# Performance work log

Hardware: AMD Instinct MI355X
Metric: run time of the kernel (lower is better)

The kernel has to match this reference:

```python
import jax, jax.numpy as jnp
import numpy as np

B, P, K = 8, 2048, 20          # graphs, points per graph, fps samples per graph
N, M = B * P, B * K            # total points, total fps points
C_IN, C_OUT = 64, 128
EPS = 1e-5                     # BatchNorm eps (torch default)


def _linear(x, W, b):
    return x @ W.T + b


def _bn(x, g, b):
    # training-mode BatchNorm1d: batch stats over rows (biased variance)
    m = jnp.mean(x, axis=0)
    v = jnp.var(x, axis=0)
    return g * (x - m) * jax.lax.rsqrt(v + EPS) + b


def _mlp(x, W1, b1, g1, be1, W2, b2, g2, be2):
    h = jax.nn.relu(_bn(_linear(x, W1, b1), g1, be1))
    return jax.nn.relu(_bn(_linear(h, W2, b2), g2, be2))


def setup_inputs() -> dict:
    key = jax.random.key(0)
    ks = jax.random.split(key, 16)
    rng = np.random.default_rng(0)
    # sorted FPS indices: 20 distinct points per graph (matches indices.sort())
    fps = np.sort(rng.choice(P, size=(B, K), replace=False), axis=1)
    fps = fps + np.arange(B)[:, None] * P

    s = 0.05
    inp = {
        "x": jax.random.normal(ks[0], (N, C_IN), jnp.float32),
        "pos": jax.random.normal(ks[1], (N, 3), jnp.float32),
        # q/k/v projections
        "Wq": jax.random.normal(ks[2], (C_OUT, C_IN)) * s, "bq": jnp.zeros((C_OUT,)),
        "Wk": jax.random.normal(ks[3], (C_OUT, C_IN)) * s, "bk": jnp.zeros((C_OUT,)),
        "Wv": jax.random.normal(ks[4], (C_OUT, C_IN)) * s, "bv": jnp.zeros((C_OUT,)),
        # pos MLP: Linear(3,C) BN ReLU Linear(C,C) BN ReLU
        "pW1": jax.random.normal(ks[5], (C_OUT, 3)) * s, "pb1": jnp.zeros((C_OUT,)),
        "pg1": jnp.ones((C_OUT,)), "pbe1": jnp.zeros((C_OUT,)),
        "pW2": jax.random.normal(ks[6], (C_OUT, C_OUT)) * s, "pb2": jnp.zeros((C_OUT,)),
        "pg2": jnp.ones((C_OUT,)), "pbe2": jnp.zeros((C_OUT,)),
        # attn MLP: Linear(C,C) BN ReLU Linear(C,C) BN ReLU
        "aW1": jax.random.normal(ks[7], (C_OUT, C_OUT)) * s, "ab1": jnp.zeros((C_OUT,)),
        "ag1": jnp.ones((C_OUT,)), "abe1": jnp.zeros((C_OUT,)),
        "aW2": jax.random.normal(ks[8], (C_OUT, C_OUT)) * s, "ab2": jnp.zeros((C_OUT,)),
        "ag2": jnp.ones((C_OUT,)), "abe2": jnp.zeros((C_OUT,)),
        "fps_idx": jnp.asarray(fps.reshape(-1), jnp.int32),
        "batch": jnp.repeat(jnp.arange(B, dtype=jnp.int32), P),
    }
    return inp


def reference(x, pos, Wq, bq, Wk, bk, Wv, bv,
              pW1, pb1, pg1, pbe1, pW2, pb2, pg2, pbe2,
              aW1, ab1, ag1, abe1, aW2, ab2, ag2, abe2,
              fps_idx, batch):
    # --- FPS gather + knn(k=1, batched) ---
    fps_pos = pos[fps_idx]                          # [M,3]
    pos_b = pos.reshape(B, P, 3)
    fpos_b = fps_pos.reshape(B, K, 3)
    d2 = jnp.sum((pos_b[:, :, None, :] - fpos_b[:, None, :, :]) ** 2, -1)  # [B,P,K]
    nn_local = jnp.argmin(d2, axis=-1)              # [B,P] nearest fps per point
    e1 = (nn_local + jnp.arange(B)[:, None] * K).reshape(-1)  # [N] global fps idx
    ek1 = 1.0 / (1.0 + 5.0 * jnp.min(d2, axis=-1).reshape(-1))  # [N]

    # --- scatter-mean of kernel-weighted x/pos onto fps nodes ---
    seg = jax.ops.segment_sum
    cnt = jnp.maximum(seg(jnp.ones((N,), x.dtype), e1, num_segments=M), 1.0)[:, None]
    fps_x = seg(ek1[:, None] * x, e1, num_segments=M) / cnt       # [M,C_IN]
    fps_pos = seg(ek1[:, None] * pos, e1, num_segments=M) / cnt   # [M,3]

    # --- q/k/v projections ---
    x_q = _linear(x, Wq, bq)        # [N,C]
    x_k = _linear(fps_x, Wk, bk)    # [M,C]
    x_v = _linear(fps_x, Wv, bv)    # [M,C]

    # --- all-pairs (local point, global fps-in-same-graph) edges: E = N*K ---
    rel = (pos_b[:, :, None, :] - fps_pos.reshape(B, K, 3)[:, None, :, :])
    rel = rel.reshape(N * K, 3)                                   # [E,3]
    delta = _mlp(rel, pW1, pb1, pg1, pbe1, pW2, pb2, pg2, pbe2)   # [E,C]

    qmk = (x_q.reshape(B, P, 1, C_OUT) - x_k.reshape(B, 1, K, C_OUT))
    qmk = qmk.reshape(N * K, C_OUT)                               # [E,C]
    alpha = _mlp(qmk + delta, aW1, ab1, ag1, abe1, aW2, ab2, ag2, abe2)
    # segment softmax over each local point's K edges, per channel
    alpha = jax.nn.softmax(alpha.reshape(B, P, K, C_OUT), axis=2)

    vpd = x_v.reshape(B, 1, K, C_OUT) + delta.reshape(B, P, K, C_OUT)
    out = jnp.sum(vpd * alpha, axis=2).reshape(N, C_OUT)          # scatter-add
    return out
```

## Files before the change

kernel.cpp:

```cpp
#include <hip/hip_runtime.h>
#include <hip/hip_bf16.h>
#include <stdint.h>

#define B_ 8
#define P_ 2048
#define K_ 20
#define N_ (B_*P_)
#define M_ (B_*K_)
#define C 128
#define E_ (N_*K_)
#define EPS_ 1e-5f

typedef unsigned short u16;
typedef unsigned int u32;
typedef __attribute__((ext_vector_type(8))) short short8;
typedef __attribute__((ext_vector_type(4))) float floatx4;

__device__ __forceinline__ float bf2f(u16 u){
    union { u32 i; float f; } v; v.i = ((u32)u) << 16; return v.f;
}
__device__ __forceinline__ u16 f2bf(float f){
    union { float f; u32 i; } v; v.f = f;
    u32 r = ((v.i >> 16) & 1u) + 0x7fffu;
    return (u16)((v.i + r) >> 16);
}
__device__ __forceinline__ u32 pkbf(float a, float b){
    union { __hip_bfloat162 h; u32 u; } cv;
    cv.h = __float22bfloat162_rn(make_float2(a, b));
    return cv.u;
}

__global__ __launch_bounds__(256)
void prep_weights(const float* __restrict__ Wq, const float* __restrict__ bq,
                  const float* __restrict__ Wk, const float* __restrict__ bk,
                  const float* __restrict__ aW1, const float* __restrict__ ab1,
                  const float* __restrict__ pW2, const float* __restrict__ aW2,
                  const float* __restrict__ Wv,
                  float* __restrict__ CqT, float* __restrict__ CkT,
                  float* __restrict__ dq, float* __restrict__ dk,
                  float* __restrict__ WvT,
                  u16* __restrict__ Wb0, u16* __restrict__ Wb1, u16* __restrict__ Wb2)
{
    int tid = threadIdx.x, blk = blockIdx.x;
    if (blk < 32) {
        int idx = blk*256 + tid; int o = idx >> 6, i = idx & 63;
        float s = 0.f;
        for (int cc = 0; cc < 128; ++cc) s = fmaf(aW1[o*128+cc], Wq[cc*64+i], s);
        CqT[i*128 + o] = s;
    } else if (blk < 64) {
        int idx = (blk-32)*256 + tid; int o = idx >> 6, i = idx & 63;
        float s = 0.f;
        for (int cc = 0; cc < 128; ++cc) s = fmaf(aW1[o*128+cc], Wk[cc*64+i], s);
        CkT[i*128 + o] = s;
    } else if (blk == 64) {
        if (tid < 128) {
            float s = ab1[tid];
            for (int cc = 0; cc < 128; ++cc) s = fmaf(aW1[tid*128+cc], bq[cc], s);
            dq[tid] = s;
        } else {
            int o = tid - 128;
            float s = 0.f;
            for (int cc = 0; cc < 128; ++cc) s = fmaf(aW1[o*128+cc], bk[cc], s);
            dk[o] = s;
        }
    } else if (blk == 68) {
        for (int idx = tid; idx < 8192; idx += 256) {
            int o = idx >> 6, i = idx & 63;
            WvT[i*128 + o] = Wv[idx];
        }
    } else {
        const float* src = (blk == 65) ? pW2 : (blk == 66) ? aW1 : aW2;
        u16* dst = (blk == 65) ? Wb0 : (blk == 66) ? Wb1 : Wb2;
        for (int s = tid; s < 2048; s += 256) {
            int ln = s & 63, ks = (s >> 6) & 3, ct = s >> 8;
            int Ls = ln & 15, qs = ln >> 4;
            const float* sp = src + (ct*16+Ls)*C + ks*32 + qs*8;
            #pragma unroll
            for (int j = 0; j < 8; ++j) dst[s*8+j] = f2bf(sp[j]);
        }
    }
}

__global__ __launch_bounds__(256)
void knn_scatter(const float* __restrict__ pos, const float* __restrict__ x,
                 const int* __restrict__ fps_idx, float* __restrict__ gacc,
                 float* __restrict__ posmom)
{
    __shared__ float fpos[K_][3];
    __shared__ float accL[K_*68];
    __shared__ int   skb[64];
    __shared__ float sek[64];
    int tid = threadIdx.x;
    int b = blockIdx.x >> 5;
    if (tid < K_*3) {
        int k = tid / 3, d = tid - k*3;
        fpos[k][d] = pos[fps_idx[b*K_+k]*3 + d];
    }
    for (int i = tid; i < K_*68; i += 256) accL[i] = 0.f;
    __syncthreads();

    int wbase = blockIdx.x*64;
    if (tid < 64) {
        int p = wbase + tid;
        float px = pos[p*3], py = pos[p*3+1], pz = pos[p*3+2];
        float best = 1e30f; int kb = 0;
        #pragma unroll
        for (int k = 0; k < K_; ++k) {
            float dx = px - fpos[k][0], dy = py - fpos[k][1], dz = pz - fpos[k][2];
            float d2 = dx*dx + dy*dy + dz*dz;
            if (d2 < best) { best = d2; kb = k; }
        }
        float ek = 1.0f / (1.0f + 5.0f*best);
        skb[tid] = kb; sek[tid] = ek;
        atomicAdd(&accL[kb*68 + 0], 1.0f);
        atomicAdd(&accL[kb*68 + 1], ek*px);
        atomicAdd(&accL[kb*68 + 2], ek*py);
        atomicAdd(&accL[kb*68 + 3], ek*pz);

        float mom[9] = {px,py,pz, px*px,px*py,px*pz, py*py,py*pz, pz*pz};
        #pragma unroll
        for (int i = 0; i < 9; ++i) {
            float v = mom[i];
            v += __shfl_xor(v,32); v += __shfl_xor(v,16); v += __shfl_xor(v,8);
            v += __shfl_xor(v,4);  v += __shfl_xor(v,2);  v += __shfl_xor(v,1);
            mom[i] = v;
        }
        if (tid == 0) {
            #pragma unroll
            for (int i = 0; i < 9; ++i) atomicAdd(&posmom[b*9+i], mom[i]);
        }
    }
    __syncthreads();

    int w = tid >> 6, lane = tid & 63;
    #pragma unroll
    for (int jj = 0; jj < 16; ++jj) {
        int j = w*16 + jj;
        int   kbj = skb[j];
        float ekj = sek[j];
        float xvv = x[(size_t)(wbase+j)*64 + lane];
        atomicAdd(&accL[kbj*68 + 4 + lane], ekj*xvv);
    }
    __syncthreads();
    for (int i = tid; i < K_*68; i += 256)
        atomicAdd(&gacc[b*K_*68 + i], accL[i]);
}

__global__ __launch_bounds__(128)
void proj_m(float* __restrict__ gacc, const float* __restrict__ CkT,
            const float* __restrict__ dk, const float* __restrict__ WvT,
            const float* __restrict__ bv, float* __restrict__ Ak2,
            float* __restrict__ xv)
{
    __shared__ float sfx[68];
    int m = blockIdx.x, o = threadIdx.x;
    if (o < 68) {
        float c = gacc[m*68];
        float inv = 1.0f / (c > 1.f ? c : 1.f);
        float vdiv = (o >= 1) ? gacc[m*68+o]*inv : c;
        sfx[o] = vdiv;
        if (o >= 1) gacc[m*68+o] = vdiv;
    }
    __syncthreads();
    float a = dk[o], v = bv[o];
    for (int i = 0; i < 64; ++i) {
        float xi = sfx[4+i];
        a = fmaf(CkT[i*128+o], xi, a);
        v = fmaf(WvT[i*128+o], xi, v);
    }
    Ak2[m*C+o] = a; xv[m*C+o] = v;
}

__global__ __launch_bounds__(256)
void bn1_prep(const float* __restrict__ gacc, const float* __restrict__ posmom,
              const float* __restrict__ pW1, const float* __restrict__ pb1,
              const float* __restrict__ pg1, const float* __restrict__ pbe1,
              float* __restrict__ w3)
{
    __shared__ float sF[8][3], sG[8][6];
    __shared__ float S1[3], S2[6];
    int t = threadIdx.x;
    if (t < 8) {
        float F0=0,F1=0,F2=0,G0=0,G1=0,G2=0,G3=0,G4=0,G5=0;
        for (int k = 0; k < K_; ++k) {
            const float* f = gacc + (t*K_+k)*68 + 1;
            float x=f[0], y=f[1], z=f[2];
            F0+=x; F1+=y; F2+=z;
            G0+=x*x; G1+=x*y; G2+=x*z; G3+=y*y; G4+=y*z; G5+=z*z;
        }
        sF[t][0]=F0; sF[t][1]=F1; sF[t][2]=F2;
        sG[t][0]=G0; sG[t][1]=G1; sG[t][2]=G2; sG[t][3]=G3; sG[t][4]=G4; sG[t][5]=G5;
    }
    __syncthreads();
    if (t == 0) {
        float s1[3]={0,0,0}, s2[6]={0,0,0,0,0,0};
        for (int b = 0; b < 8; ++b) {
            const float* pm = posmom + b*9;
            float Ax=pm[0],Ay=pm[1],Az=pm[2];
            float Fx=sF[b][0],Fy=sF[b][1],Fz=sF[b][2];
            s1[0] += (float)K_*Ax - (float)P_*Fx;
            s1[1] += (float)K_*Ay - (float)P_*Fy;
            s1[2] += (float)K_*Az - (float)P_*Fz;
            s2[0] += (float)K_*pm[3] - 2.f*Ax*Fx + (float)P_*sG[b][0];
            s2[1] += (float)K_*pm[4] - Ax*Fy - Ay*Fx + (float)P_*sG[b][1];
            s2[2] += (float)K_*pm[5] - Ax*Fz - Az*Fx + (float)P_*sG[b][2];
            s2[3] += (float)K_*pm[6] - 2.f*Ay*Fy + (float)P_*sG[b][3];
            s2[4] += (float)K_*pm[7] - Ay*Fz - Az*Fy + (float)P_*sG[b][4];
            s2[5] += (float)K_*pm[8] - 2.f*Az*Fz + (float)P_*sG[b][5];
        }
        for (int i = 0; i < 3; ++i) S1[i] = s1[i];
        for (int i = 0; i < 6; ++i) S2[i] = s2[i];
    }
    __syncthreads();
    if (t < 128) {
        float w0=pW1[t*3], w1=pW1[t*3+1], w2=pW1[t*3+2], bb=pb1[t];
        float wS1 = w0*S1[0] + w1*S1[1] + w2*S1[2];
        float wS2w = w0*w0*S2[0] + w1*w1*S2[3] + w2*w2*S2[5]
                   + 2.f*(w0*w1*S2[1] + w0*w2*S2[2] + w1*w2*S2[4]);
        const float invE = 1.0f/(float)E_;
        float m1  = wS1*invE + bb;
        float Ez2 = (wS2w + 2.f*bb*wS1)*invE + bb*bb;
        float var = Ez2 - m1*m1;
        float sc = pg1[t] * rsqrtf(var + EPS_);
        float sh = pbe1[t] - m1*sc;
        w3[0*128+t] = w0*sc; w3[1*128+t] = w1*sc;
        w3[2*128+t] = w2*sc; w3[3*128+t] = bb*sc + sh;
    }
}

__global__ __launch_bounds__(256)
void proj_q(const float* __restrict__ x, const float* __restrict__ CqT,
            const float* __restrict__ dq, float* __restrict__ Aq2)
{
    __shared__ float xs[512];
    int tid = threadIdx.x;
    int p0 = blockIdx.x*8;
    const float* xp = x + (size_t)p0*64;
    for (int i = tid; i < 512; i += 256) xs[i] = xp[i];
    __syncthreads();
    int g = tid >> 7, o = tid & 127;
    const float* xb = xs + g*256;
    float d = dq[o];
    float a0=d, a1=d, a2=d, a3=d;
    #pragma unroll 4
    for (int i = 0; i < 64; ++i) {
        float w = CqT[i*128 + o];
        a0 = fmaf(w, xb[i],       a0);
        a1 = fmaf(w, xb[64+i],    a1);
        a2 = fmaf(w, xb[128+i],   a2);
        a3 = fmaf(w, xb[192+i],   a3);
    }
    int pb = p0 + g*4;
    Aq2[(size_t)(pb+0)*C + o] = a0;
    Aq2[(size_t)(pb+1)*C + o] = a1;
    Aq2[(size_t)(pb+2)*C + o] = a2;
    Aq2[(size_t)(pb+3)*C + o] = a3;
}

template<int MODE>
__global__ __launch_bounds__(256)
void gemm_fused(const u16* __restrict__ zin, u16* __restrict__ zout,
                const u16* __restrict__ Wbf,
                const float* __restrict__ statsin, const float* __restrict__ g,
                const float* __restrict__ be,
                const float* __restrict__ w3, const float* __restrict__ bias,
                const float* __restrict__ rowq, const float* __restrict__ rowk,
                const float* __restrict__ pos, const float* __restrict__ gacc,
                float* __restrict__ stats32)
{
    __shared__ float s_stat[2][C];
    __shared__ float saff[5*C];

    int tid = threadIdx.x;
    const int wave = tid >> 6, lane = tid & 63;
    const int L = lane & 15, q = lane >> 4;

    ((float*)s_stat)[tid] = 0.f;
    if constexpr (MODE == 0) {
        for (int i = tid; i < 512; i += 256) saff[i] = w3[i];
        if (tid < C) saff[512+tid] = bias[tid];
    } else {
        if (tid < C) {
            float s = 0.f, sq = 0.f;
            for (int r = 0; r < 32; ++r) {
                s  += statsin[r*256 + tid];
                sq += statsin[r*256 + 128 + tid];
            }
            float mean = s*(1.0f/E_), var = sq*(1.0f/E_) - mean*mean;
            float sc = g[tid] * rsqrtf(var + EPS_);
            saff[tid] = sc; saff[C+tid] = be[tid] - mean*sc;
        }
        if constexpr (MODE == 2) {
            if (tid >= 128) saff[2*C + tid - 128] = bias[tid - 128];
        }
    }
    __syncthreads();

    int tbs[2];
    tbs[0] = (blockIdx.x*8 + wave)*16;
    tbs[1] = (blockIdx.x*8 + wave + 4)*16;

    short8 An[2][4];
    float rr0[2], rr1[2], rr2[2];
    #pragma unroll
    for (int tt = 0; tt < 2; ++tt) {
        if constexpr (MODE != 0) {
            const u16* ap = zin + (size_t)(tbs[tt] + L)*C + q*8;
            An[tt][0] = *(const short8*)ap;
            An[tt][1] = *(const short8*)(ap + 32);
            An[tt][2] = *(const short8*)(ap + 64);
            An[tt][3] = *(const short8*)(ap + 96);
        } else {
            unsigned e = (unsigned)(tbs[tt] + L);
            unsigned p = e / 20u; int k = (int)(e - p*20u);
            int m = (int)(p >> 11)*20 + k;
            const float* fp = gacc + m*68 + 1;
            rr0[tt] = pos[p*3]   - fp[0];
            rr1[tt] = pos[p*3+1] - fp[1];
            rr2[tt] = pos[p*3+2] - fp[2];
        }
    }

    floatx4 acc[2][8];
    #pragma unroll
    for (int tt = 0; tt < 2; ++tt)
        #pragma unroll
        for (int ct = 0; ct < 8; ++ct) acc[tt][ct] = (floatx4){0.f,0.f,0.f,0.f};

    #pragma unroll
    for (int ks = 0; ks < 4; ++ks) {
        int ch0 = ks*32 + q*8;
        short8 bfr[8];
        #pragma unroll
        for (int ct = 0; ct < 8; ++ct)
            bfr[ct] = *(const short8*)(Wbf + ((ct*4+ks)*64 + lane)*8);
        #pragma unroll
        for (int tt = 0; tt < 2; ++tt) {
            union { short8 s8; u32 u[4]; } af;
            if constexpr (MODE == 0) {
                #pragma unroll
                for (int jj = 0; jj < 4; ++jj) {
                    int c0 = ch0 + jj*2, c1 = ch0 + jj*2 + 1;
                    float f0 = fmaf(saff[c0], rr0[tt], fmaf(saff[C+c0], rr1[tt],
                               fmaf(saff[2*C+c0], rr2[tt], saff[3*C+c0])));
                    float f1 = fmaf(saff[c1], rr0[tt], fmaf(saff[C+c1], rr1[tt],
                               fmaf(saff[2*C+c1], rr2[tt], saff[3*C+c1])));
                    f0 = f0 > 0.f ? f0 : 0.f;
                    f1 = f1 > 0.f ? f1 : 0.f;
                    af.u[jj] = pkbf(f0, f1);
                }
            } else {
                short8 ar = An[tt][ks];
                #pragma unroll
                for (int jj = 0; jj < 4; ++jj) {
                    int c0 = ch0 + jj*2, c1 = ch0 + jj*2 + 1;
                    float f0 = fmaf(bf2f((u16)ar[jj*2]),   saff[c0], saff[C+c0]);
                    float f1 = fmaf(bf2f((u16)ar[jj*2+1]), saff[c1], saff[C+c1]);
                    f0 = f0 > 0.f ? f0 : 0.f;
                    f1 = f1 > 0.f ? f1 : 0.f;
                    af.u[jj] = pkbf(f0, f1);
                }
            }
            #pragma unroll
            for (int ct = 0; ct < 8; ++ct)
                acc[tt][ct] = __builtin_amdgcn_mfma_f32_16x16x32_bf16(af.s8, bfr[ct], acc[tt][ct], 0, 0, 0);
        }
    }

    float ssum[8], ssq[8];
    #pragma unroll
    for (int i = 0; i < 8; ++i) { ssum[i] = 0.f; ssq[i] = 0.f; }

    #pragma unroll
    for (int tt = 0; tt < 2; ++tt) {
        const int tilebase = tbs[tt];
        int pp[4], mm[4];
        if constexpr (MODE == 1) {
            #pragma unroll
            for (int r = 0; r < 4; ++r) {
                unsigned e2 = (unsigned)(tilebase + q*4 + r);
                unsigned p2 = e2 / 20u; int k2 = (int)(e2 - p2*20u);
                pp[r] = (int)p2; mm[r] = (int)(p2 >> 11)*20 + k2;
            }
        }
        u16* orow = zout + (size_t)(tilebase + q*4)*C + L;
        #pragma unroll
        for (int ct = 0; ct < 8; ++ct) {
            int col = ct*16 + L;
            float bb;
            if constexpr (MODE == 0) bb = saff[4*C + col];
            else if constexpr (MODE == 2) bb = saff[2*C + col];
            else bb = 0.f;
            #pragma unroll
            for (int r = 0; r < 4; ++r) {
                float z = acc[tt][ct][r] + bb;
                if constexpr (MODE == 1)
                    z += rowq[pp[r]*C + col] - rowk[mm[r]*C + col];
                ssum[ct] += z; ssq[ct] += z*z;
                orow[(size_t)r*C + ct*16] = (u16)pkbf(z, z);
            }
        }
    }

    #pragma unroll
    for (int ct = 0; ct < 8; ++ct) {
        float v = ssum[ct]; v += __shfl_xor(v,16); v += __shfl_xor(v,32);
        float w = ssq[ct];  w += __shfl_xor(w,16); w += __shfl_xor(w,32);
        if (lane < 16) {
            atomicAdd(&s_stat[0][ct*16+L], v);
            atomicAdd(&s_stat[1][ct*16+L], w);
        }
    }
    __syncthreads();
    float* dst = stats32 + ((blockIdx.x & 31) << 8);
    atomicAdd(&dst[tid], ((float*)s_stat)[tid]);
}

__global__ __launch_bounds__(256)
void final_kernel(const u16* __restrict__ z2, const u16* __restrict__ za2,
                  const float* __restrict__ stA, const float* __restrict__ pg2,
                  const float* __restrict__ pbe2,
                  const float* __restrict__ stC, const float* __restrict__ ag2,
                  const float* __restrict__ abe2,
                  const float* __restrict__ xv, float* __restrict__ out)
{
    __shared__ float saff[4*C];
    int tid = threadIdx.x;
    if (tid < C) {
        float s=0.f, sq=0.f;
        for (int r = 0; r < 32; ++r) { s += stA[r*256+tid]; sq += stA[r*256+128+tid]; }
        float mean = s*(1.0f/E_), var = sq*(1.0f/E_)-mean*mean;
        float sc = pg2[tid]*rsqrtf(var+EPS_);
        saff[tid] = sc; saff[C+tid] = pbe2[tid]-mean*sc;
    } else {
        int c = tid - C;
        float s=0.f, sq=0.f;
        for (int r = 0; r < 32; ++r) { s += stC[r*256+c]; sq += stC[r*256+128+c]; }
        float mean = s*(1.0f/E_), var = sq*(1.0f/E_)-mean*mean;
        float sc = ag2[c]*rsqrtf(var+EPS_);
        saff[2*C+c] = sc; saff[3*C+c] = abe2[c]-mean*sc;
    }
    __syncthreads();

    int wave = tid >> 6, lane = tid & 63;
    int p0 = blockIdx.x*8 + wave*2;
    int c2 = lane*2;
    int b = p0 >> 11;
    float S2x=saff[c2], S2y=saff[c2+1], H2x=saff[C+c2], H2y=saff[C+c2+1];
    float S4x=saff[2*C+c2], S4y=saff[2*C+c2+1], H4x=saff[3*C+c2], H4y=saff[3*C+c2+1];
    size_t eb0 = (size_t)p0 * K_;
    size_t eb1 = eb0 + K_;
    const float* xvb = xv + (size_t)(b*K_)*C + c2;
    float l0a=0.f, l1a=0.f, o0a=0.f, o1a=0.f;
    float l0b=0.f, l1b=0.f, o0b=0.f, o1b=0.f;
    #pragma unroll
    for (int k = 0; k < K_; ++k) {
        u32 waA = *(const u32*)(za2 + (eb0+k)*C + c2);
        u32 wzA = *(const u32*)(z2  + (eb0+k)*C + c2);
        u32 waB = *(const u32*)(za2 + (eb1+k)*C + c2);
        u32 wzB = *(const u32*)(z2  + (eb1+k)*C + c2);
        float2 xvv = *(const float2*)(xvb + (size_t)k*C);
        float aa0 = fmaf(bf2f((u16)(waA & 0xffffu)), S4x, H4x); aa0 = aa0 > 0.f ? aa0 : 0.f;
        float aa1 = fmaf(bf2f((u16)(waA >> 16)),     S4y, H4y); aa1 = aa1 > 0.f ? aa1 : 0.f;
        float dd0 = fmaf(bf2f((u16)(wzA & 0xffffu)), S2x, H2x); dd0 = dd0 > 0.f ? dd0 : 0.f;
        float dd1 = fmaf(bf2f((u16)(wzA >> 16)),     S2y, H2y); dd1 = dd1 > 0.f ? dd1 : 0.f;
        float e0 = __expf(aa0), e1 = __expf(aa1);
        l0a += e0; l1a += e1;
        o0a = fmaf(e0, xvv.x + dd0, o0a);
        o1a = fmaf(e1, xvv.y + dd1, o1a);
        float ba0 = fmaf(bf2f((u16)(waB & 0xffffu)), S4x, H4x); ba0 = ba0 > 0.f ? ba0 : 0.f;
        float ba1 = fmaf(bf2f((u16)(waB >> 16)),     S4y, H4y); ba1 = ba1 > 0.f ? ba1 : 0.f;
        float bd0 = fmaf(bf2f((u16)(wzB & 0xffffu)), S2x, H2x); bd0 = bd0 > 0.f ? bd0 : 0.f;
        float bd1 = fmaf(bf2f((u16)(wzB >> 16)),     S2y, H2y); bd1 = bd1 > 0.f ? bd1 : 0.f;
        float f0 = __expf(ba0), f1 = __expf(ba1);
        l0b += f0; l1b += f1;
        o0b = fmaf(f0, xvv.x + bd0, o0b);
        o1b = fmaf(f1, xvv.y + bd1, o1b);
    }
    out[(size_t)p0*C + c2]       = o0a / l0a;
    out[(size_t)p0*C + c2 + 1]   = o1a / l1a;
    out[(size_t)(p0+1)*C + c2]     = o0b / l0b;
    out[(size_t)(p0+1)*C + c2 + 1] = o1b / l1b;
}

extern "C" void kernel_launch(void* const* d_in, const int* in_sizes, int n_in,
                              void* d_out, int out_size, void* d_ws, size_t ws_size,
                              hipStream_t stream)
{
    const float* x    = (const float*)d_in[0];
    const float* pos  = (const float*)d_in[1];
    const float* Wq   = (const float*)d_in[2];
    const float* bq   = (const float*)d_in[3];
    const float* Wk   = (const float*)d_in[4];
    const float* bk   = (const float*)d_in[5];
    const float* Wv   = (const float*)d_in[6];
    const float* bv   = (const float*)d_in[7];
    const float* pW1  = (const float*)d_in[8];
    const float* pb1  = (const float*)d_in[9];
    const float* pg1  = (const float*)d_in[10];
    const float* pbe1 = (const float*)d_in[11];
    const float* pW2  = (const float*)d_in[12];
    const float* pb2  = (const float*)d_in[13];
    const float* pg2  = (const float*)d_in[14];
    const float* pbe2 = (const float*)d_in[15];
    const float* aW1  = (const float*)d_in[16];
    const float* ab1  = (const float*)d_in[17];
    const float* ag1  = (const float*)d_in[18];
    const float* abe1 = (const float*)d_in[19];
    const float* aW2  = (const float*)d_in[20];
    const float* ab2  = (const float*)d_in[21];
    const float* ag2  = (const float*)d_in[22];
    const float* abe2 = (const float*)d_in[23];
    const int* fps_idx = (const int*)d_in[24];
    float* out = (float*)d_out;

    char* ws = (char*)d_ws;
    size_t off = 0;
    auto alloc = [&](size_t bytes) -> void* {
        void* r = ws + off;
        off = (off + bytes + 255) & ~(size_t)255;
        return r;
    };
    float* gacc    = (float*)alloc(160*68*4);
    float* posmom  = (float*)alloc(8*9*4);
    float* stats32 = (float*)alloc(3*32*256*4);
    size_t zero_bytes = off;
    float* w3  = (float*)alloc(4*128*4);
    float* CqT = (float*)alloc(64*128*4);
    float* CkT = (float*)alloc(64*128*4);
    float* dq  = (float*)alloc(128*4);
    float* dk  = (float*)alloc(128*4);
    float* WvT = (float*)alloc(64*128*4);
    u16* Wb0   = (u16*)alloc(128*128*2);
    u16* Wb1   = (u16*)alloc(128*128*2);
    u16* Wb2   = (u16*)alloc(128*128*2);
    float* Aq2 = (float*)alloc((size_t)N_*128*4);
    float* Ak2 = (float*)alloc(160*128*4);
    float* xv  = (float*)alloc(160*128*4);
    u16* bigA  = (u16*)alloc((size_t)E_*128*2);
    u16* bigB  = (u16*)alloc((size_t)E_*128*2);

    hipMemsetAsync(d_ws, 0, zero_bytes, stream);

    prep_weights<<<69, 256, 0, stream>>>(Wq, bq, Wk, bk, aW1, ab1, pW2, aW2, Wv,
                                         CqT, CkT, dq, dk, WvT, Wb0, Wb1, Wb2);
    knn_scatter<<<256, 256, 0, stream>>>(pos, x, fps_idx, gacc, posmom);
    proj_m<<<160, 128, 0, stream>>>(gacc, CkT, dk, WvT, bv, Ak2, xv);
    bn1_prep<<<1, 256, 0, stream>>>(gacc, posmom, pW1, pb1, pg1, pbe1, w3);
    proj_q<<<N_/8, 256, 0, stream>>>(x, CqT, dq, Aq2);

    float* stA = stats32;
    float* stB = stats32 + 32*256;
    float* stC = stats32 + 2*32*256;

    gemm_fused<0><<<E_/128, 256, 0, stream>>>(nullptr, bigA, Wb0,
        nullptr, nullptr, nullptr, w3, pb2, nullptr, nullptr, pos, gacc, stA);

    gemm_fused<1><<<E_/128, 256, 0, stream>>>(bigA, bigB, Wb1,
        stA, pg2, pbe2, nullptr, nullptr, Aq2, Ak2, nullptr, nullptr, stB);

    gemm_fused<2><<<E_/128, 256, 0, stream>>>(bigB, bigB, Wb2,
        stB, ag1, abe1, nullptr, ab2, nullptr, nullptr, nullptr, nullptr, stC);

    final_kernel<<<N_/8, 256, 0, stream>>>(bigA, bigB,
        stA, pg2, pbe2, stC, ag2, abe2, xv, out);
}
```

Measured before the change: 326.4 us.

## Permute weight output columns so each lane stores 8 contiguous bf16 outputs

Reorders the packed bf16 weight layout so MFMA output tile ct/lane L maps to output channel L*8+ct. Each lane then holds 8 consecutive channels per row, which allows 16-byte vector stores of the z outputs, vectorized bias loads and vectorized rowq/rowk gathers, in place of scattered 2-byte stores. Per-channel stat accumulation indices are remapped to match. Correctness depends on every consumer of Wb0/Wb1/Wb2 agreeing with the new column permutation.

```diff
diff --git a/kernel.cpp b/kernel.cpp
--- a/kernel.cpp
+++ b/kernel.cpp
@@ -74,7 +74,7 @@
         for (int s = tid; s < 2048; s += 256) {
             int ln = s & 63, ks = (s >> 6) & 3, ct = s >> 8;
             int Ls = ln & 15, qs = ln >> 4;
-            const float* sp = src + (ct*16+Ls)*C + ks*32 + qs*8;
+            const float* sp = src + (Ls*8 + ct)*C + ks*32 + qs*8;
             #pragma unroll
             for (int j = 0; j < 8; ++j) dst[s*8+j] = f2bf(sp[j]);
         }
@@ -383,32 +383,48 @@
                 pp[r] = (int)p2; mm[r] = (int)(p2 >> 11)*20 + k2;
             }
         }
-        u16* orow = zout + (size_t)(tilebase + q*4)*C + L;
+        u16* orow = zout + (size_t)(tilebase + q*4)*C + L*8;
+        floatx4 bb0, bb1;
+        if constexpr (MODE == 0) {
+            bb0 = *(const floatx4*)&saff[4*C + L*8];
+            bb1 = *(const floatx4*)&saff[4*C + L*8 + 4];
+        } else if constexpr (MODE == 2) {
+            bb0 = *(const floatx4*)&saff[2*C + L*8];
+            bb1 = *(const floatx4*)&saff[2*C + L*8 + 4];
+        }
         #pragma unroll
-        for (int ct = 0; ct < 8; ++ct) {
-            int col = ct*16 + L;
-            float bb;
-            if constexpr (MODE == 0) bb = saff[4*C + col];
-            else if constexpr (MODE == 2) bb = saff[2*C + col];
-            else bb = 0.f;
+        for (int r = 0; r < 4; ++r) {
+            floatx4 z0, z1;
             #pragma unroll
-            for (int r = 0; r < 4; ++r) {
-                float z = acc[tt][ct][r] + bb;
-                if constexpr (MODE == 1)
-                    z += rowq[pp[r]*C + col] - rowk[mm[r]*C + col];
-                ssum[ct] += z; ssq[ct] += z*z;
-                orow[(size_t)r*C + ct*16] = (u16)pkbf(z, z);
+            for (int j = 0; j < 4; ++j) { z0[j] = acc[tt][j][r]; z1[j] = acc[tt][4+j][r]; }
+            if constexpr (MODE == 0 || MODE == 2) { z0 += bb0; z1 += bb1; }
+            if constexpr (MODE == 1) {
+                const float* rq = &rowq[pp[r]*C + L*8];
+                const float* rk = &rowk[mm[r]*C + L*8];
+                z0 += *(const floatx4*)rq - *(const floatx4*)rk;
+                z1 += *(const floatx4*)(rq+4) - *(const floatx4*)(rk+4);
             }
-        }
-    }
-
-    #pragma unroll
-    for (int ct = 0; ct < 8; ++ct) {
-        float v = ssum[ct]; v += __shfl_xor(v,16); v += __shfl_xor(v,32);
-        float w = ssq[ct];  w += __shfl_xor(w,16); w += __shfl_xor(w,32);
+            #pragma unroll
+            for (int j = 0; j < 4; ++j) {
+                ssum[j]   += z0[j]; ssq[j]   += z0[j]*z0[j];
+                ssum[4+j] += z1[j]; ssq[4+j] += z1[j]*z1[j];
+            }
+            union { short8 s8; u32 u[4]; } ov;
+            ov.u[0] = pkbf(z0[0], z0[1]);
+            ov.u[1] = pkbf(z0[2], z0[3]);
+            ov.u[2] = pkbf(z1[0], z1[1]);
+            ov.u[3] = pkbf(z1[2], z1[3]);
+            *(short8*)(orow + (size_t)r*C) = ov.s8;
+        }
+    }
+
+    #pragma unroll
+    for (int j = 0; j < 8; ++j) {
+        float v = ssum[j]; v += __shfl_xor(v,16); v += __shfl_xor(v,32);
+        float w = ssq[j];  w += __shfl_xor(w,16); w += __shfl_xor(w,32);
         if (lane < 16) {
-            atomicAdd(&s_stat[0][ct*16+L], v);
-            atomicAdd(&s_stat[1][ct*16+L], w);
+            atomicAdd(&s_stat[0][lane*8+j], v);
+            atomicAdd(&s_stat[1][lane*8+j], w);
         }
     }
     __syncthreads();
```

Result: faster. 313.8 us (-3.9%).
